# Kernel tuning notes

Hardware: AMD Instinct MI355X
Metric: run time of the kernel (lower is better)

The kernel has to match this reference:

```python
import jax, jax.numpy as jnp
import numpy as np

N_QUBITS = 4
N_LAYERS = 2
BATCH = 524288


def _ry(theta):
    # RY(theta) = [[cos(t/2), -sin(t/2)], [sin(t/2), cos(t/2)]], shape [..., 2, 2]
    c = jnp.cos(theta / 2)
    s = jnp.sin(theta / 2)
    return jnp.stack([jnp.stack([c, -s], -1), jnp.stack([s, c], -1)], -2).astype(jnp.complex64)


def _rz(theta):
    # RZ(theta) = diag(exp(-i t/2), exp(i t/2))
    p = jnp.exp(-1j * theta / 2)
    pc = jnp.exp(1j * theta / 2)
    z = jnp.zeros_like(p)
    return jnp.stack([jnp.stack([p, z], -1), jnp.stack([z, pc], -1)], -2).astype(jnp.complex64)


def _apply_1q(state, gate, q):
    # state: [B,2,2,2,2] (axis 1+q is qubit q, wire 0 most significant as in default.qubit)
    # gate: [2,2] (shared) or [B,2,2] (per-sample)
    letters = list('abcd')
    t = letters[q]
    out = letters.copy()
    out[q] = 'z'
    if gate.ndim == 3:
        sub = f"Bz{t},B{''.join(letters)}->B{''.join(out)}"
    else:
        sub = f"z{t},B{''.join(letters)}->B{''.join(out)}"
    return jnp.einsum(sub, gate, state)


def _cnot(state, c, t):
    # flip target axis on the control=1 slice
    s0 = jnp.take(state, 0, axis=1 + c)
    s1 = jnp.take(state, 1, axis=1 + c)
    ta = 1 + t - (1 if t > c else 0)
    s1 = jnp.flip(s1, axis=ta)
    return jnp.stack([s0, s1], axis=1 + c)


def _circuit(x, weights):
    B = x.shape[0]
    state = jnp.zeros((B, 2, 2, 2, 2), jnp.complex64).at[:, 0, 0, 0, 0].set(1.0)
    ry_in = _ry(x)  # [B, 4, 2, 2], per-sample input encoding
    for q in range(N_QUBITS):
        state = _apply_1q(state, ry_in[:, q], q)
    for l in range(N_LAYERS):
        for q in range(N_QUBITS):
            state = _apply_1q(state, _rz(weights[l, q, 0]), q)
            state = _apply_1q(state, _ry(weights[l, q, 1]), q)
        for q in range(N_QUBITS - 1):
            state = _cnot(state, q, q + 1)
        state = _cnot(state, N_QUBITS - 1, 0)
    probs = jnp.abs(state.reshape(B, 16)) ** 2
    # <Z_i> = sum_s p(s) * (1 - 2*bit_i(s)); wire 0 is the most significant bit
    bits = (np.arange(16)[:, None] >> np.arange(N_QUBITS - 1, -1, -1)) & 1
    signs = jnp.asarray(1.0 - 2.0 * bits, jnp.float32)  # [16, 4]
    return probs @ signs  # [B, 4]


def setup_inputs() -> dict:
    key = jax.random.key(0)
    k1, k2 = jax.random.split(key)
    x = jax.random.normal(k1, (BATCH, N_QUBITS), dtype=jnp.float32)
    # TorchLayer default init: uniform in [0, 2*pi)
    weights = jax.random.uniform(k2, (N_LAYERS, N_QUBITS, 2), dtype=jnp.float32, minval=0.0, maxval=2 * np.pi)
    return {"x": x, "weights": weights}


def reference(x, weights):
    return _circuit(x, weights)
```

## Files before the change

kernel.cpp:

```cpp
#include <hip/hip_runtime.h>

#define BATCH 524288
#define NQ 4
#define TPB 256
#define V 2

__global__ __launch_bounds__(TPB, 2) void qlayer_kernel(const float* __restrict__ x,
                                                        const float* __restrict__ w,
                                                        float* __restrict__ out) {
    __shared__ float Ure[16][16];
    __shared__ float Uim[16][16];

    const int tid = threadIdx.x;

    if (tid < 16) {
        float stx[16], sty[16];
        #pragma unroll
        for (int i = 0; i < 16; i++) { stx[i] = 0.f; sty[i] = 0.f; }
        stx[tid] = 1.f;

        #pragma unroll
        for (int l = 0; l < 2; l++) {
            #pragma unroll
            for (int q = 0; q < 4; q++) {
                float cz, sz, cy, sy;
                __sincosf(0.5f * w[l * 8 + q * 2 + 0], &sz, &cz);
                __sincosf(0.5f * w[l * 8 + q * 2 + 1], &sy, &cy);
                const int mask = 8 >> q;
                #pragma unroll
                for (int i = 0; i < 16; i++) {
                    float ax = stx[i], ay = sty[i];
                    if (i & mask) { stx[i] = ax * cz - ay * sz; sty[i] = ay * cz + ax * sz; }
                    else          { stx[i] = ax * cz + ay * sz; sty[i] = ay * cz - ax * sz; }
                }
                #pragma unroll
                for (int i = 0; i < 16; i++) {
                    if (!(i & mask)) {
                        float a0x = stx[i], a0y = sty[i];
                        float a1x = stx[i | mask], a1y = sty[i | mask];
                        stx[i]        = cy * a0x - sy * a1x;
                        sty[i]        = cy * a0y - sy * a1y;
                        stx[i | mask] = sy * a0x + cy * a1x;
                        sty[i | mask] = sy * a0y + cy * a1y;
                    }
                }
            }
            #pragma unroll
            for (int e = 0; e < 4; e++) {
                const int cqs[4] = {0, 1, 2, 3};
                const int tqs[4] = {1, 2, 3, 0};
                const int cm = 8 >> cqs[e];
                const int tm = 8 >> tqs[e];
                #pragma unroll
                for (int i = 0; i < 16; i++) {
                    if ((i & cm) && !(i & tm)) {
                        float t0x = stx[i], t0y = sty[i];
                        stx[i] = stx[i | tm]; sty[i] = sty[i | tm];
                        stx[i | tm] = t0x;    sty[i | tm] = t0y;
                    }
                }
            }
        }
        #pragma unroll
        for (int j = 0; j < 16; j++) { Ure[j][tid] = stx[j]; Uim[j][tid] = sty[j]; }
    }
    __syncthreads();

    const int base = blockIdx.x * (TPB * V) + tid;

    float sv[V][16];
    #pragma unroll
    for (int v = 0; v < V; v++) {
        const int smp = base + v * TPB;
        const float4 xv = reinterpret_cast<const float4*>(x)[smp];
        float c0, s0, c1, s1, c2, s2, c3, s3;
        __sincosf(0.5f * xv.x, &s0, &c0);
        __sincosf(0.5f * xv.y, &s1, &c1);
        __sincosf(0.5f * xv.z, &s2, &c2);
        __sincosf(0.5f * xv.w, &s3, &c3);
        const float p01[4] = {c0 * c1, c0 * s1, s0 * c1, s0 * s1};
        const float p23[4] = {c2 * c3, c2 * s3, s2 * c3, s2 * s3};
        #pragma unroll
        for (int i = 0; i < 16; i++) sv[v][i] = p01[i >> 2] * p23[i & 3];
    }

    float z[V][4];
    #pragma unroll
    for (int v = 0; v < V; v++)
        #pragma unroll
        for (int i = 0; i < 4; i++) z[v][i] = 0.f;

    #pragma unroll
    for (int j = 0; j < 16; j++) {
        float urow[16], irow[16];
        #pragma unroll
        for (int kk = 0; kk < 4; kk++) {
            const float4 a = reinterpret_cast<const float4*>(&Ure[j][0])[kk];
            const float4 b = reinterpret_cast<const float4*>(&Uim[j][0])[kk];
            urow[4 * kk + 0] = a.x; urow[4 * kk + 1] = a.y;
            urow[4 * kk + 2] = a.z; urow[4 * kk + 3] = a.w;
            irow[4 * kk + 0] = b.x; irow[4 * kk + 1] = b.y;
            irow[4 * kk + 2] = b.z; irow[4 * kk + 3] = b.w;
        }
        #pragma unroll
        for (int v = 0; v < V; v++) {
            float re = 0.f, im = 0.f;
            #pragma unroll
            for (int k = 0; k < 16; k++) {
                re = fmaf(urow[k], sv[v][k], re);
                im = fmaf(irow[k], sv[v][k], im);
            }
            const float p = re * re + im * im;
            z[v][0] += (j & 8) ? -p : p;
            z[v][1] += (j & 4) ? -p : p;
            z[v][2] += (j & 2) ? -p : p;
            z[v][3] += (j & 1) ? -p : p;
        }
    }

    #pragma unroll
    for (int v = 0; v < V; v++) {
        const int smp = base + v * TPB;
        reinterpret_cast<float4*>(out)[smp] = make_float4(z[v][0], z[v][1], z[v][2], z[v][3]);
    }
}

extern "C" void kernel_launch(void* const* d_in, const int* in_sizes, int n_in,
                              void* d_out, int out_size, void* d_ws, size_t ws_size,
                              hipStream_t stream) {
    const float* x = (const float*)d_in[0];
    const float* w = (const float*)d_in[1];
    float* out = (float*)d_out;
    const int grid = BATCH / (TPB * V);
    qlayer_kernel<<<grid, TPB, 0, stream>>>(x, w, out);
}
```

Baseline: 72.82 us.

## Split unitary construction into a prep kernel and read it from global memory

The 16x16 circuit unitary is now built once by a separate single-block prep kernel and written to workspace, instead of being rebuilt by 16 threads in every block with a shared-memory barrier. The main kernel reads the unitary through uniform global loads, which can become scalar loads, and drops the shared-memory staging. Launch bounds are raised to allow more waves per SIMD. The cost is an extra kernel launch and a serialized dependency between the two kernels.

```diff
diff --git a/kernel.cpp b/kernel.cpp
--- a/kernel.cpp
+++ b/kernel.cpp
@@ -1,72 +1,71 @@
 #include <hip/hip_runtime.h>
 
 #define BATCH 524288
-#define NQ 4
 #define TPB 256
 #define V 2
 
-__global__ __launch_bounds__(TPB, 2) void qlayer_kernel(const float* __restrict__ x,
-                                                        const float* __restrict__ w,
-                                                        float* __restrict__ out) {
-    __shared__ float Ure[16][16];
-    __shared__ float Uim[16][16];
+__global__ void qprep_kernel(const float* __restrict__ w, float* __restrict__ ws) {
+    const int tid = threadIdx.x;
+    if (tid >= 16) return;
 
-    const int tid = threadIdx.x;
+    float stx[16], sty[16];
+    #pragma unroll
+    for (int i = 0; i < 16; i++) { stx[i] = 0.f; sty[i] = 0.f; }
+    stx[tid] = 1.f;
 
-    if (tid < 16) {
-        float stx[16], sty[16];
+    #pragma unroll
+    for (int l = 0; l < 2; l++) {
         #pragma unroll
-        for (int i = 0; i < 16; i++) { stx[i] = 0.f; sty[i] = 0.f; }
-        stx[tid] = 1.f;
-
-        #pragma unroll
-        for (int l = 0; l < 2; l++) {
+        for (int q = 0; q < 4; q++) {
+            float cz, sz, cy, sy;
+            __sincosf(0.5f * w[l * 8 + q * 2 + 0], &sz, &cz);
+            __sincosf(0.5f * w[l * 8 + q * 2 + 1], &sy, &cy);
+            const int mask = 8 >> q;
             #pragma unroll
-            for (int q = 0; q < 4; q++) {
-                float cz, sz, cy, sy;
-                __sincosf(0.5f * w[l * 8 + q * 2 + 0], &sz, &cz);
-                __sincosf(0.5f * w[l * 8 + q * 2 + 1], &sy, &cy);
-                const int mask = 8 >> q;
-                #pragma unroll
-                for (int i = 0; i < 16; i++) {
-                    float ax = stx[i], ay = sty[i];
-                    if (i & mask) { stx[i] = ax * cz - ay * sz; sty[i] = ay * cz + ax * sz; }
-                    else          { stx[i] = ax * cz + ay * sz; sty[i] = ay * cz - ax * sz; }
-                }
-                #pragma unroll
-                for (int i = 0; i < 16; i++) {
-                    if (!(i & mask)) {
-                        float a0x = stx[i], a0y = sty[i];
-                        float a1x = stx[i | mask], a1y = sty[i | mask];
-                        stx[i]        = cy * a0x - sy * a1x;
-                        sty[i]        = cy * a0y - sy * a1y;
-                        stx[i | mask] = sy * a0x + cy * a1x;
-                        sty[i | mask] = sy * a0y + cy * a1y;
-                    }
-                }
+            for (int i = 0; i < 16; i++) {
+                float ax = stx[i], ay = sty[i];
+                if (i & mask) { stx[i] = ax * cz - ay * sz; sty[i] = ay * cz + ax * sz; }
+                else          { stx[i] = ax * cz + ay * sz; sty[i] = ay * cz - ax * sz; }
             }
             #pragma unroll
-            for (int e = 0; e < 4; e++) {
-                const int cqs[4] = {0, 1, 2, 3};
-                const int tqs[4] = {1, 2, 3, 0};
-                const int cm = 8 >> cqs[e];
-                const int tm = 8 >> tqs[e];
-                #pragma unroll
-                for (int i = 0; i < 16; i++) {
-                    if ((i & cm) && !(i & tm)) {
-                        float t0x = stx[i], t0y = sty[i];
-                        stx[i] = stx[i | tm]; sty[i] = sty[i | tm];
-                        stx[i | tm] = t0x;    sty[i | tm] = t0y;
-                    }
+            for (int i = 0; i < 16; i++) {
+                if (!(i & mask)) {
+                    float a0x = stx[i], a0y = sty[i];
+                    float a1x = stx[i | mask], a1y = sty[i | mask];
+                    stx[i]        = cy * a0x - sy * a1x;
+                    sty[i]        = cy * a0y - sy * a1y;
+                    stx[i | mask] = sy * a0x + cy * a1x;
+                    sty[i | mask] = sy * a0y + cy * a1y;
                 }
             }
         }
         #pragma unroll
-        for (int j = 0; j < 16; j++) { Ure[j][tid] = stx[j]; Uim[j][tid] = sty[j]; }
+        for (int e = 0; e < 4; e++) {
+            const int cqs[4] = {0, 1, 2, 3};
+            const int tqs[4] = {1, 2, 3, 0};
+            const int cm = 8 >> cqs[e];
+            const int tm = 8 >> tqs[e];
+            #pragma unroll
+            for (int i = 0; i < 16; i++) {
+                if ((i & cm) && !(i & tm)) {
+                    float t0x = stx[i], t0y = sty[i];
+                    stx[i] = stx[i | tm]; sty[i] = sty[i | tm];
+                    stx[i | tm] = t0x;    sty[i | tm] = t0y;
+                }
+            }
+        }
     }
-    __syncthreads();
+    #pragma unroll
+    for (int j = 0; j < 16; j++) {
+        ws[j * 32 + tid]      = stx[j];
+        ws[j * 32 + 16 + tid] = sty[j];
+    }
+}
 
-    const int base = blockIdx.x * (TPB * V) + tid;
+__global__ __launch_bounds__(TPB, 4) void qmain_kernel(const float* __restrict__ x,
+                                                       const float* __restrict__ U,
+                                                       float* __restrict__ out) {
+    const int base = blockIdx.x * (TPB * V) + threadIdx.x;
 
     float sv[V][16];
     #pragma unroll
@@ -92,25 +91,22 @@
 
     #pragma unroll
     for (int j = 0; j < 16; j++) {
-        float urow[16], irow[16];
+        float re[V], im[V];
         #pragma unroll
-        for (int kk = 0; kk < 4; kk++) {
-            const float4 a = reinterpret_cast<const float4*>(&Ure[j][0])[kk];
-            const float4 b = reinterpret_cast<const float4*>(&Uim[j][0])[kk];
-            urow[4 * kk + 0] = a.x; urow[4 * kk + 1] = a.y;
-            urow[4 * kk + 2] = a.z; urow[4 * kk + 3] = a.w;
-            irow[4 * kk + 0] = b.x; irow[4 * kk + 1] = b.y;
-            irow[4 * kk + 2] = b.z; irow[4 * kk + 3] = b.w;
+        for (int v = 0; v < V; v++) { re[v] = 0.f; im[v] = 0.f; }
+        #pragma unroll
+        for (int k = 0; k < 16; k++) {
+            const float ur = U[j * 32 + k];
+            const float ui = U[j * 32 + 16 + k];
+            #pragma unroll
+            for (int v = 0; v < V; v++) {
+                re[v] = fmaf(ur, sv[v][k], re[v]);
+                im[v] = fmaf(ui, sv[v][k], im[v]);
+            }
         }
         #pragma unroll
         for (int v = 0; v < V; v++) {
-            float re = 0.f, im = 0.f;
-            #pragma unroll
-            for (int k = 0; k < 16; k++) {
-                re = fmaf(urow[k], sv[v][k], re);
-                im = fmaf(irow[k], sv[v][k], im);
-            }
-            const float p = re * re + im * im;
+            const float p = re[v] * re[v] + im[v] * im[v];
             z[v][0] += (j & 8) ? -p : p;
             z[v][1] += (j & 4) ? -p : p;
             z[v][2] += (j & 2) ? -p : p;
@@ -131,6 +127,9 @@
     const float* x = (const float*)d_in[0];
     const float* w = (const float*)d_in[1];
     float* out = (float*)d_out;
+    float* U = (float*)d_ws;
+
+    qprep_kernel<<<1, 64, 0, stream>>>(w, U);
     const int grid = BATCH / (TPB * V);
-    qlayer_kernel<<<grid, TPB, 0, stream>>>(x, w, out);
+    qmain_kernel<<<grid, TPB, 0, stream>>>(x, U, out);
 }
```

Result: faster. 69.24 us (-4.9%).
